# Performance work log

Hardware: AMD Instinct MI355X
Metric: run time of the kernel (lower is better)

## Reference

```python
import jax, jax.numpy as jnp
import numpy as np

BN_EPS = 1e-4  # KAIR BatchNorm2d eps


def conv1x1(x, W, b):
    # x: (b,c,h,w), W: (out,in), b: (out,)
    return jnp.einsum('oc,bchw->bohw', W, x) + b[None, :, None, None]


def setup_inputs() -> dict:
    key = jax.random.key(0)
    ks = jax.random.split(key, 16)
    b, c, h, w = 8, 64, 128, 128
    f32 = jnp.float32

    def rn(k, shape, s=0.05):
        return jax.random.normal(k, shape, f32) * s

    c3 = 3 * c
    return {
        'x': jax.random.normal(ks[0], (b, c, h, w), f32),
        'xf': jax.random.normal(ks[1], (b, c, h, w), f32),
        'xr': jax.random.normal(ks[2], (b, c, h, w), f32),
        'Wx': rn(ks[3], (c, c)), 'bx': jnp.zeros((c,), f32),
        'Wx1': rn(ks[4], (c, c)), 'bx1': jnp.zeros((c,), f32),
        'Wx2': rn(ks[5], (c, c)), 'bx2': jnp.zeros((c,), f32),
        'Wxf': rn(ks[6], (c, c)), 'bxf': jnp.zeros((c,), f32),
        'Wxr': rn(ks[7], (c, c)), 'bxr': jnp.zeros((c,), f32),
        'W_msa': rn(ks[8], (c3, c3, 3, 3)), 'b_msa': jnp.zeros((c3,), f32),
        'bn_gamma': jnp.ones((c3,), f32), 'bn_beta': jnp.zeros((c3,), f32),
        'bn_mean': jnp.zeros((c3,), f32), 'bn_var': jnp.ones((c3,), f32),
    }


def reference(x, xf, xr, Wx, bx, Wx1, bx1, Wx2, bx2, Wxf, bxf, Wxr, bxr,
              W_msa, b_msa, bn_gamma, bn_beta, bn_mean, bn_var):
    x_org = x
    # 1x1 conv projections (note: x1/x2 are projections of the projected x)
    xp = conv1x1(x, Wx, bx)
    x1 = conv1x1(xp, Wx1, bx1)
    x2 = conv1x1(xp, Wx2, bx2)
    xfp = conv1x1(xf, Wxf, bxf)
    xrp = conv1x1(xr, Wxr, bxr)

    # score1 = rearrange(x1,'b c h w->b h c w') @ rearrange(xf,'b c h w->b h w c') -> (b,h,c,c)
    score1 = jnp.einsum('bchw,bdhw->bhcd', x1, xfp)
    # feature_xf = score1 @ rearrange(x,'b c h w->b h c w'), rearranged back to (b,c,h,w)
    feature_xf = jnp.einsum('bhcd,bdhw->bchw', score1, xp)
    score2 = jnp.einsum('bchw,bdhw->bhcd', x2, xrp)
    feature_xr = jnp.einsum('bhcd,bdhw->bchw', score2, xp)

    out = jnp.concatenate([feature_xf, feature_xr, x_org], axis=1)  # (b,3c,h,w)
    # msa_conv: Conv2d(3c,3c,3,s=1,p=1) + BatchNorm2d(eval) + ReLU
    out = jax.lax.conv_general_dilated(
        out, W_msa, window_strides=(1, 1), padding='SAME',
        dimension_numbers=('NCHW', 'OIHW', 'NCHW'))
    out = out + b_msa[None, :, None, None]
    inv = jax.lax.rsqrt(bn_var + BN_EPS)
    out = (out - bn_mean[None, :, None, None]) * (bn_gamma * inv)[None, :, None, None] \
          + bn_beta[None, :, None, None]
    return jax.nn.relu(out)
```

## Files before the change

kernel.cpp:

```cpp
#include <hip/hip_runtime.h>

#define BATCH 8
#define C     64
#define H     128
#define WD    128
#define C3    192
#define HW    (H*WD)
#define PW    130
#define CBUF  (4*PW*64)

#define SWZ(r) ((((r) & 7) ^ (((r) >> 3) & 6)))

typedef __attribute__((ext_vector_type(8))) short short8;
typedef __attribute__((ext_vector_type(4))) float f32x4;
typedef unsigned short ushort_t;

__device__ __forceinline__ unsigned short f2bf(float f) {
    unsigned u = __builtin_bit_cast(unsigned, f);
    u += 0x7fffu + ((u >> 16) & 1u);
    return (unsigned short)(u >> 16);
}
__device__ __forceinline__ int pack2(unsigned short lo, unsigned short hi) {
    return (int)(((unsigned)hi << 16) | (unsigned)lo);
}

__global__ __launch_bounds__(64) void compose_kernel(
    const float* __restrict__ Wx,  const float* __restrict__ bx,
    const float* __restrict__ Wx1, const float* __restrict__ bx1,
    const float* __restrict__ Wx2, const float* __restrict__ bx2,
    const float* __restrict__ Wxf, const float* __restrict__ bxf,
    const float* __restrict__ Wxr, const float* __restrict__ bxr,
    ushort_t* __restrict__ Wall, float* __restrict__ ball)
{
    int o = blockIdx.x;
    int c = threadIdx.x;
    Wall[0*4096 + o*64 + c] = f2bf(Wx [o*64 + c]);
    Wall[3*4096 + o*64 + c] = f2bf(Wxf[o*64 + c]);
    Wall[4*4096 + o*64 + c] = f2bf(Wxr[o*64 + c]);
    float a1 = 0.f, a2 = 0.f;
    for (int k = 0; k < 64; ++k) {
        float wc = Wx[k*64 + c];
        a1 += Wx1[o*64 + k] * wc;
        a2 += Wx2[o*64 + k] * wc;
    }
    Wall[1*4096 + o*64 + c] = f2bf(a1);
    Wall[2*4096 + o*64 + c] = f2bf(a2);
    float t1 = Wx1[o*64 + c] * bx[c];
    float t2 = Wx2[o*64 + c] * bx[c];
    for (int off = 32; off; off >>= 1) {
        t1 += __shfl_down(t1, off);
        t2 += __shfl_down(t2, off);
    }
    if (c == 0) {
        ball[0*64 + o] = bx[o];
        ball[1*64 + o] = bx1[o] + t1;
        ball[2*64 + o] = bx2[o] + t2;
        ball[3*64 + o] = bxf[o];
        ball[4*64 + o] = bxr[o];
    }
}

__global__ __launch_bounds__(256) void prep_kernel(
    const float* __restrict__ x, const float* __restrict__ xf,
    const float* __restrict__ xr,
    ushort_t* __restrict__ xcl, ushort_t* __restrict__ feat,
    ushort_t* __restrict__ xfT, ushort_t* __restrict__ xrT)
{
    const int which = blockIdx.x / (BATCH*PW);
    const int r = blockIdx.x % (BATCH*PW);
    const int b = r / PW, py = r % PW;
    const int t = threadIdx.x;
    const size_t prow = ((size_t)b*PW + py)*PW;

    __shared__ ushort_t sx[128*72];

    if (which == 0) {
        if (py == 0 || py == PW-1) {
            int4 z = make_int4(0,0,0,0);
            for (int j = t; j < PW*128/8; j += 256) ((int4*)(feat + prow*128))[j] = z;
            for (int j = t; j < PW*64/8;  j += 256) ((int4*)(xcl  + prow*64 ))[j] = z;
            return;
        }
        if (t < 48) {
            int4 z = make_int4(0,0,0,0);
            if (t < 32) {
                int side = t >> 4, seg = t & 15;
                *(int4*)(feat + (prow + (side ? PW-1 : 0))*128 + seg*8) = z;
            } else {
                int u = t - 32, side = u >> 3, seg = u & 7;
                *(int4*)(xcl + (prow + (side ? PW-1 : 0))*64 + seg*8) = z;
            }
        }
        const int y = py - 1;
        for (int k = t; k < 64*128; k += 256) {
            int c = k >> 7, xx = k & 127;
            sx[xx*72 + c] = f2bf(x[((size_t)b*C + c)*HW + (size_t)y*WD + xx]);
        }
        __syncthreads();
        for (int j = t; j < 128*8; j += 256) {
            int xx = j >> 3, seg = j & 7;
            *(int4*)(xcl + (prow + xx + 1)*64 + seg*8) = *(const int4*)(sx + xx*72 + seg*8);
        }
        return;
    }

    if (py == 0 || py == PW-1) return;
    const int y = py - 1;
    const float* src = (which == 1) ? xf : xr;
    ushort_t* dstT   = (which == 1) ? xfT : xrT;
    for (int k = t; k < 64*128; k += 256) {
        int c = k >> 7, xx = k & 127;
        sx[xx*72 + c] = f2bf(src[((size_t)b*C + c)*HW + (size_t)y*WD + xx]);
    }
    __syncthreads();
    for (int j = t; j < 128*8; j += 256) {
        int xx = j >> 3, seg = j & 7;
        *(int4*)(dstT + (((size_t)b*128 + y)*128 + xx)*64 + seg*8) = *(const int4*)(sx + xx*72 + seg*8);
    }
}

__global__ __launch_bounds__(256, 3) void attn_mfma(
    const ushort_t* __restrict__ xcl, const ushort_t* __restrict__ xfT,
    const ushort_t* __restrict__ xrT,
    const ushort_t* __restrict__ Wall, const float* __restrict__ ball,
    ushort_t* __restrict__ feat)
{
    __shared__ ushort_t lds[6*4096];
    ushort_t* P = lds;
    ushort_t* Q = lds + 4096;
    ushort_t* U = lds + 2*4096;
    ushort_t* R = lds + 3*4096;
    ushort_t* V = lds + 4*4096;
    ushort_t* T = lds + 5*4096;

    const int t = threadIdx.x;
    const int wv = t >> 6, lane = t & 63, m = lane & 15, quad = lane >> 4;
    const int b = blockIdx.x >> 7, h = blockIdx.x & 127;
    const size_t rowbase = ((size_t)b*PW + h + 1)*PW;
    const ushort_t* xrow  = xcl + (rowbase + 1)*64;
    const ushort_t* xfrow = xfT + ((size_t)b*128 + h)*128*64;
    const ushort_t* xrrow = xrT + ((size_t)b*128 + h)*128*64;

    auto stageT = [&](const ushort_t* base, ushort_t* dst) {
#pragma unroll
        for (int it = 0; it < 2; ++it) {
            int slot = it*256 + t;
            int w = slot >> 3, seg = slot & 7;
            *(int4*)(dst + w*64 + ((seg ^ SWZ(w)) << 3)) =
                *(const int4*)(base + w*64 + seg*8);
        }
    };
    auto projB = [&](const ushort_t* src, const ushort_t* W, const float* bias,
                     ushort_t* dst) {
        int arow = wv*16 + m;
        int sa = SWZ(arow);
#pragma unroll
        for (int nt = 0; nt < 4; ++nt) {
            f32x4 acc = {0.f,0.f,0.f,0.f};
#pragma unroll
            for (int k = 0; k < 2; ++k) {
                short8 a  = *(const short8*)(src + arow*64 + (((4*k+quad) ^ sa) << 3));
                short8 bb = *(const short8*)(W   + (nt*16 + m)*64  + k*32 + quad*8);
                acc = __builtin_amdgcn_mfma_f32_16x16x32_bf16(a, bb, acc, 0,0,0);
            }
            float bo = bias[nt*16 + m];
            int o = nt*16 + m, w0 = wv*16 + quad*4;
            int base = o*64 + (((w0 >> 3) ^ SWZ(o)) << 3) + (w0 & 7);
            *(int*)(dst + base)     = pack2(f2bf(acc[0]+bo), f2bf(acc[1]+bo));
            *(int*)(dst + base + 2) = pack2(f2bf(acc[2]+bo), f2bf(acc[3]+bo));
        }
    };
    auto projA = [&](const ushort_t* src, const ushort_t* W, const float* bias,
                     ushort_t* dstT) {
        float b4[4];
#pragma unroll
        for (int r = 0; r < 4; ++r) b4[r] = bias[wv*16 + quad*4 + r];
#pragma unroll
        for (int nt = 0; nt < 4; ++nt) {
            f32x4 acc = {0.f,0.f,0.f,0.f};
            int brow = nt*16 + m;
            int sb = SWZ(brow);
#pragma unroll
            for (int k = 0; k < 2; ++k) {
                short8 a  = *(const short8*)(W   + (wv*16 + m)*64  + k*32 + quad*8);
                short8 bb = *(const short8*)(src + brow*64 + (((4*k+quad) ^ sb) << 3));
                acc = __builtin_amdgcn_mfma_f32_16x16x32_bf16(a, bb, acc, 0,0,0);
            }
            int w = nt*16 + m, o0 = wv*16 + quad*4;
            int base = w*64 + (((o0 >> 3) ^ SWZ(w)) << 3) + (o0 & 7);
            *(int*)(dstT + base)     = pack2(f2bf(acc[0]+b4[0]), f2bf(acc[1]+b4[1]));
            *(int*)(dstT + base + 2) = pack2(f2bf(acc[2]+b4[2]), f2bf(acc[3]+b4[3]));
        }
    };
    auto scoreStep = [&](const ushort_t* A, const ushort_t* B, f32x4* sc) {
        int arow = wv*16 + m;
        int sa = SWZ(arow);
#pragma unroll
        for (int nt = 0; nt < 4; ++nt) {
            int brow = nt*16 + m;
            int sb = SWZ(brow);
#pragma unroll
            for (int k = 0; k < 2; ++k) {
                short8 a  = *(const short8*)(A + arow*64 + (((4*k+quad) ^ sa) << 3));
                short8 bb = *(const short8*)(B + brow*64 + (((4*k+quad) ^ sb) << 3));
                sc[nt] = __builtin_amdgcn_mfma_f32_16x16x32_bf16(a, bb, sc[nt], 0,0,0);
            }
        }
    };
    auto scoreDump = [&](const f32x4* sc, ushort_t* dst) {
        int c0 = wv*16 + quad*4;
#pragma unroll
        for (int nt = 0; nt < 4; ++nt) {
            int d = nt*16 + m;
            int gd = d >> 3, dl = d & 7;
#pragma unroll
            for (int r = 0; r < 4; ++r) {
                int row = c0 + r;
                dst[row*64 + ((gd ^ SWZ(row)) << 3) + dl] = f2bf(sc[nt][r]);
            }
        }
    };
    auto featF = [&](const ushort_t* Sc, const ushort_t* XpT, ushort_t* stg) {
        int arow = wv*16 + m;
        int sa = SWZ(arow);
#pragma unroll
        for (int nt = 0; nt < 4; ++nt) {
            f32x4 acc = {0.f,0.f,0.f,0.f};
            int brow = nt*16 + m;
            int sb = SWZ(brow);
#pragma unroll
            for (int k = 0; k < 2; ++k) {
                short8 a  = *(const short8*)(Sc  + arow*64 + (((4*k+quad) ^ sa) << 3));
                short8 bb = *(const short8*)(XpT + brow*64 + (((4*k+quad) ^ sb) << 3));
                acc = __builtin_amdgcn_mfma_f32_16x16x32_bf16(a, bb, acc, 0,0,0);
            }
            int w = nt*16 + m, c0 = wv*16 + quad*4;
            int base = w*64 + (((c0 >> 3) ^ SWZ(w)) << 3) + (c0 & 7);
            *(int*)(stg + base)     = pack2(f2bf(acc[0]), f2bf(acc[1]));
            *(int*)(stg + base + 2) = pack2(f2bf(acc[2]), f2bf(acc[3]));
        }
    };
    auto emitPair = [&](const ushort_t* O1, const ushort_t* O2, int wc) {
#pragma unroll
        for (int it = 0; it < 4; ++it) {
            int j = (it & 1)*256 + t;
            const ushort_t* S = (it < 2) ? O1 : O2;
            int half = (it < 2) ? 0 : 64;
            int row = j >> 3, seg = j & 7;
            int4 v = *(const int4*)(S + row*64 + ((seg ^ SWZ(row)) << 3));
            *(int4*)(feat + (rowbase + wc + 1 + row)*128 + half + seg*8) = v;
        }
    };

    const ushort_t* W0 = Wall;            const float* b0 = ball;
    const ushort_t* W1 = Wall + 4096;     const float* b1 = ball + 64;
    const ushort_t* W2 = Wall + 2*4096;   const float* b2 = ball + 128;
    const ushort_t* W3 = Wall + 3*4096;   const float* b3 = ball + 192;
    const ushort_t* W4 = Wall + 4*4096;   const float* b4 = ball + 256;

    f32x4 sc1[4], sc2[4];
#pragma unroll
    for (int i = 0; i < 4; ++i) { sc1[i] = (f32x4){0,0,0,0}; sc2[i] = (f32x4){0,0,0,0}; }

    stageT(xrow, P); stageT(xfrow, Q); stageT(xrrow, U);
    __syncthreads();
    projB(P, W1, b1, R);  projB(P, W2, b2, V);  projB(Q, W3, b3, T);
    __syncthreads();
    scoreStep(R, T, sc1); projB(U, W4, b4, Q);
    __syncthreads();
    scoreStep(V, Q, sc2);
    stageT(xrow + 64*64, P); stageT(xfrow + 64*64, T); stageT(xrrow + 64*64, U);
    __syncthreads();
    projB(P, W1, b1, R);  projB(P, W2, b2, V);  projB(T, W3, b3, Q);
    __syncthreads();
    scoreStep(R, Q, sc1); projB(U, W4, b4, T);
    __syncthreads();
    scoreStep(V, T, sc2);
    stageT(xrow, P);
    __syncthreads();

    scoreDump(sc1, Q);  scoreDump(sc2, U);
    __syncthreads();
    projA(P, W0, b0, R);
    __syncthreads();
    featF(Q, R, P);  featF(U, R, T);  stageT(xrow + 64*64, V);
    __syncthreads();
    emitPair(P, T, 0);
    __syncthreads();
    projA(V, W0, b0, R);
    __syncthreads();
    featF(Q, R, V);  featF(U, R, T);
    __syncthreads();
    emitPair(V, T, 64);
}

__global__ __launch_bounds__(256) void pack_kernel(const float* __restrict__ W,
                                                   ushort_t* __restrict__ Wpk)
{
    int k = blockIdx.x*256 + threadIdx.x;
    if (k >= 12*54*64) return;
    int lane = k & 63, os = k >> 6;
    int otile = os / 54, s = os % 54;
    int tap = s / 6, icc = s % 6;
    int o   = otile*16 + (lane & 15);
    int ic0 = icc*32 + (lane >> 4)*8;
    ushort_t v[8];
#pragma unroll
    for (int j = 0; j < 8; ++j)
        v[j] = f2bf(W[(size_t)(o*C3 + ic0 + j)*9 + tap]);
    *(int4*)(Wpk + (size_t)k*8) = *(const int4*)v;
}

__global__ __launch_bounds__(512, 2) void conv_mfma(
    const ushort_t* __restrict__ feat, const ushort_t* __restrict__ xcl,
    const ushort_t* __restrict__ Wpk,
    const float* __restrict__ bias, const float* __restrict__ gamma,
    const float* __restrict__ beta, const float* __restrict__ mean,
    const float* __restrict__ var,  float* __restrict__ out)
{
    __shared__ ushort_t sA[2*CBUF];

    const int t = threadIdx.x;
    const int wv = t >> 6, lane = t & 63;
    const int m = lane & 15, quad = lane >> 4;
    const int b  = blockIdx.x >> 6, y0 = (blockIdx.x & 63)*2;
    const int yi = wv & 1, og = wv >> 1;

    f32x4 acc[24];
#pragma unroll
    for (int i = 0; i < 24; ++i) acc[i] = (f32x4){0.f,0.f,0.f,0.f};

    auto stageAll = [&](int ch, int bufi) {
        ushort_t* dst = sA + bufi*CBUF;
        const ushort_t* base = (ch < 2) ? feat : xcl;
        const int ps = (ch < 2) ? 128 : 64;
        const int co = (ch == 1) ? 64 : 0;
#pragma unroll
        for (int i = 0; i < 8; ++i) {
            int sl = i*512 + t;
            int wi = sl & 7, rowgx = sl >> 3;
            int row = rowgx / PW, gx = rowgx - row*PW;
            int wl = wi ^ (gx & 7);
            const ushort_t* g = base + (((size_t)b*PW + y0 + row)*PW + gx)*ps
                                     + co + wl*8;
            __builtin_amdgcn_global_load_lds(
                (const __attribute__((address_space(1))) unsigned int*)g,
                (__attribute__((address_space(3))) unsigned int*)(dst + (size_t)sl*8),
                16, 0, 0);
        }
        if (t < 64) {
            int sl = 4096 + t;
            int wi = sl & 7, rowgx = sl >> 3;
            int row = rowgx / PW, gx = rowgx - row*PW;
            int wl = wi ^ (gx & 7);
            const ushort_t* g = base + (((size_t)b*PW + y0 + row)*PW + gx)*ps
                                     + co + wl*8;
            __builtin_amdgcn_global_load_lds(
                (const __attribute__((address_space(1))) unsigned int*)g,
                (__attribute__((address_space(3))) unsigned int*)(dst + (size_t)sl*8),
                16, 0, 0);
        }
    };

    auto compute = [&](int ch, int bufi) {
        const ushort_t* src = sA + bufi*CBUF;
        short8 bf[6], bfn[6];
#pragma unroll
        for (int j = 0; j < 3; ++j)
#pragma unroll
            for (int k = 0; k < 2; ++k)
                bf[j*2+k] = *(const short8*)(Wpk +
                    (((size_t)(og*3+j)*54 + ch*2 + k)*64 + lane)*8);
#pragma unroll
        for (int tap = 0; tap < 9; ++tap) {
            if (tap < 8) {
#pragma unroll
                for (int j = 0; j < 3; ++j)
#pragma unroll
                    for (int k = 0; k < 2; ++k)
                        bfn[j*2+k] = *(const short8*)(Wpk +
                            (((size_t)(og*3+j)*54 + (tap+1)*6 + ch*2 + k)*64 + lane)*8);
            }
            const int ky = tap/3, kx = tap - ky*3;
            const int sw = (kx + m) & 7;
            const int rowb = ((yi + ky)*PW + kx + m)*64;
            const int g0 = (quad ^ sw)*8, g1 = ((quad+4) ^ sw)*8;
#pragma unroll
            for (int xt = 0; xt < 8; ++xt) {
                short8 af0 = *(const short8*)(src + rowb + xt*1024 + g0);
                short8 af1 = *(const short8*)(src + rowb + xt*1024 + g1);
#pragma unroll
                for (int j = 0; j < 3; ++j) {
                    acc[j*8+xt] = __builtin_amdgcn_mfma_f32_16x16x32_bf16(af0, bf[j*2],   acc[j*8+xt], 0,0,0);
                    acc[j*8+xt] = __builtin_amdgcn_mfma_f32_16x16x32_bf16(af1, bf[j*2+1], acc[j*8+xt], 0,0,0);
                }
            }
#pragma unroll
            for (int q = 0; q < 6; ++q) bf[q] = bfn[q];
        }
    };

    stageAll(0, 0);
    __syncthreads();
    for (int ch = 0; ch < 3; ++ch) {
        if (ch < 2) stageAll(ch + 1, (ch + 1) & 1);
        compute(ch, ch & 1);
        __syncthreads();
    }

    float* sOut = (float*)sA;
    for (int y = 0; y < 2; ++y) {
        if (yi == y) {
#pragma unroll
            for (int j = 0; j < 3; ++j) {
                int o = (og*3 + j)*16 + m;
                float A  = gamma[o] * rsqrtf(var[o] + 1e-4f);
                float Bv = (bias[o] - mean[o])*A + beta[o];
#pragma unroll
                for (int xt = 0; xt < 8; ++xt) {
                    f32x4 a4 = acc[j*8 + xt];
                    *(float4*)(sOut + o*132 + xt*16 + quad*4) =
                        make_float4(fmaxf(a4[0]*A + Bv, 0.f), fmaxf(a4[1]*A + Bv, 0.f),
                                    fmaxf(a4[2]*A + Bv, 0.f), fmaxf(a4[3]*A + Bv, 0.f));
                }
            }
        }
        __syncthreads();
#pragma unroll
        for (int i = 0; i < 12; ++i) {
            int s = i*512 + t;
            int o = s >> 5, xs4 = (s & 31)*4;
            float4 v = *(const float4*)(sOut + o*132 + xs4);
            *(float4*)(out + (((size_t)b*C3 + o)*H + y0 + y)*WD + xs4) = v;
        }
        __syncthreads();
    }
}

extern "C" void kernel_launch(void* const* d_in, const int* in_sizes, int n_in,
                              void* d_out, int out_size, void* d_ws, size_t ws_size,
                              hipStream_t stream)
{
    const float* x   = (const float*)d_in[0];
    const float* xf  = (const float*)d_in[1];
    const float* xr  = (const float*)d_in[2];
    const float* Wx  = (const float*)d_in[3];
    const float* bx  = (const float*)d_in[4];
    const float* Wx1 = (const float*)d_in[5];
    const float* bx1 = (const float*)d_in[6];
    const float* Wx2 = (const float*)d_in[7];
    const float* bx2 = (const float*)d_in[8];
    const float* Wxf = (const float*)d_in[9];
    const float* bxf = (const float*)d_in[10];
    const float* Wxr = (const float*)d_in[11];
    const float* bxr = (const float*)d_in[12];
    const float* Wm  = (const float*)d_in[13];
    const float* bms = (const float*)d_in[14];
    const float* gam = (const float*)d_in[15];
    const float* bet = (const float*)d_in[16];
    const float* mea = (const float*)d_in[17];
    const float* va  = (const float*)d_in[18];
    (void)in_sizes; (void)n_in; (void)out_size; (void)ws_size;

    ushort_t* feat = (ushort_t*)d_ws;
    ushort_t* xcl  = (ushort_t*)((char*)d_ws + 34611200);
    ushort_t* Wpk  = (ushort_t*)((char*)d_ws + 51916800);
    ushort_t* Wall = (ushort_t*)((char*)d_ws + 52700000);
    float*    ball = (float*)   ((char*)d_ws + 52750000);
    ushort_t* xfT  = (ushort_t*)d_out;
    ushort_t* xrT  = (ushort_t*)((char*)d_out + 16777216);
    float* outp = (float*)d_out;

    compose_kernel<<<dim3(64), dim3(64), 0, stream>>>(
        Wx, bx, Wx1, bx1, Wx2, bx2, Wxf, bxf, Wxr, bxr, Wall, ball);
    pack_kernel<<<dim3(162), dim3(256), 0, stream>>>(Wm, Wpk);
    prep_kernel<<<dim3(3*BATCH*PW), dim3(256), 0, stream>>>(
        x, xf, xr, xcl, feat, xfT, xrT);
    attn_mfma<<<dim3(BATCH*H), dim3(256), 0, stream>>>(
        xcl, xfT, xrT, Wall, ball, feat);
    conv_mfma<<<dim3(BATCH*64), dim3(512), 0, stream>>>(
        feat, xcl, Wpk, bms, gam, bet, mea, va, outp);
}
```

Before: 356.8 us.

## Split conv row tile into two x-halves to halve accumulators and LDS

The 3x3 conv MFMA kernel now processes each two-row tile in two 64-column halves. Each half stages a smaller halo buffer and keeps 12 accumulator vectors instead of 24. This cuts register and LDS use per block so more waves can be resident. In exchange, weights are reloaded twice per block, halo columns are restaged, and there are more barriers.

```diff
diff --git a/kernel.cpp b/kernel.cpp
--- a/kernel.cpp
+++ b/kernel.cpp
@@ -7,7 +7,8 @@
 #define C3    192
 #define HW    (H*WD)
 #define PW    130
-#define CBUF  (4*PW*64)
+#define HGX   66
+#define HBUF  (4*HGX*64)
 
 #define SWZ(r) ((((r) & 7) ^ (((r) >> 3) & 6)))
 
@@ -318,7 +319,7 @@
     const float* __restrict__ beta, const float* __restrict__ mean,
     const float* __restrict__ var,  float* __restrict__ out)
 {
-    __shared__ ushort_t sA[2*CBUF];
+    __shared__ ushort_t sA[2*HBUF];
 
     const int t = threadIdx.x;
     const int wv = t >> 6, lane = t & 63;
@@ -326,22 +327,20 @@
     const int b  = blockIdx.x >> 6, y0 = (blockIdx.x & 63)*2;
     const int yi = wv & 1, og = wv >> 1;
 
-    f32x4 acc[24];
-#pragma unroll
-    for (int i = 0; i < 24; ++i) acc[i] = (f32x4){0.f,0.f,0.f,0.f};
-
-    auto stageAll = [&](int ch, int bufi) {
-        ushort_t* dst = sA + bufi*CBUF;
+    f32x4 acc[12];
+
+    auto stageH = [&](int ch, int xh, int bufi) {
+        ushort_t* dst = sA + bufi*HBUF;
         const ushort_t* base = (ch < 2) ? feat : xcl;
         const int ps = (ch < 2) ? 128 : 64;
         const int co = (ch == 1) ? 64 : 0;
 #pragma unroll
-        for (int i = 0; i < 8; ++i) {
+        for (int i = 0; i < 4; ++i) {
             int sl = i*512 + t;
             int wi = sl & 7, rowgx = sl >> 3;
-            int row = rowgx / PW, gx = rowgx - row*PW;
-            int wl = wi ^ (gx & 7);
-            const ushort_t* g = base + (((size_t)b*PW + y0 + row)*PW + gx)*ps
+            int row = rowgx / HGX, gxl = rowgx - row*HGX;
+            int wl = wi ^ (gxl & 7);
+            const ushort_t* g = base + (((size_t)b*PW + y0 + row)*PW + xh*64 + gxl)*ps
                                      + co + wl*8;
             __builtin_amdgcn_global_load_lds(
                 (const __attribute__((address_space(1))) unsigned int*)g,
@@ -349,11 +348,11 @@
                 16, 0, 0);
         }
         if (t < 64) {
-            int sl = 4096 + t;
+            int sl = 2048 + t;
             int wi = sl & 7, rowgx = sl >> 3;
-            int row = rowgx / PW, gx = rowgx - row*PW;
-            int wl = wi ^ (gx & 7);
-            const ushort_t* g = base + (((size_t)b*PW + y0 + row)*PW + gx)*ps
+            int row = rowgx / HGX, gxl = rowgx - row*HGX;
+            int wl = wi ^ (gxl & 7);
+            const ushort_t* g = base + (((size_t)b*PW + y0 + row)*PW + xh*64 + gxl)*ps
                                      + co + wl*8;
             __builtin_amdgcn_global_load_lds(
                 (const __attribute__((address_space(1))) unsigned int*)g,
@@ -363,7 +362,7 @@
     };
 
     auto compute = [&](int ch, int bufi) {
-        const ushort_t* src = sA + bufi*CBUF;
+        const ushort_t* src = sA + bufi*HBUF;
         short8 bf[6], bfn[6];
 #pragma unroll
         for (int j = 0; j < 3; ++j)
@@ -383,16 +382,16 @@
             }
             const int ky = tap/3, kx = tap - ky*3;
             const int sw = (kx + m) & 7;
-            const int rowb = ((yi + ky)*PW + kx + m)*64;
+            const int rowb = ((yi + ky)*HGX + kx + m)*64;
             const int g0 = (quad ^ sw)*8, g1 = ((quad+4) ^ sw)*8;
 #pragma unroll
-            for (int xt = 0; xt < 8; ++xt) {
-                short8 af0 = *(const short8*)(src + rowb + xt*1024 + g0);
-                short8 af1 = *(const short8*)(src + rowb + xt*1024 + g1);
+            for (int xtl = 0; xtl < 4; ++xtl) {
+                short8 af0 = *(const short8*)(src + rowb + xtl*1024 + g0);
+                short8 af1 = *(const short8*)(src + rowb + xtl*1024 + g1);
 #pragma unroll
                 for (int j = 0; j < 3; ++j) {
-                    acc[j*8+xt] = __builtin_amdgcn_mfma_f32_16x16x32_bf16(af0, bf[j*2],   acc[j*8+xt], 0,0,0);
-                    acc[j*8+xt] = __builtin_amdgcn_mfma_f32_16x16x32_bf16(af1, bf[j*2+1], acc[j*8+xt], 0,0,0);
+                    acc[j*4+xtl] = __builtin_amdgcn_mfma_f32_16x16x32_bf16(af0, bf[j*2],   acc[j*4+xtl], 0,0,0);
+                    acc[j*4+xtl] = __builtin_amdgcn_mfma_f32_16x16x32_bf16(af1, bf[j*2+1], acc[j*4+xtl], 0,0,0);
                 }
             }
 #pragma unroll
@@ -400,40 +399,43 @@
         }
     };
 
-    stageAll(0, 0);
-    __syncthreads();
-    for (int ch = 0; ch < 3; ++ch) {
-        if (ch < 2) stageAll(ch + 1, (ch + 1) & 1);
-        compute(ch, ch & 1);
-        __syncthreads();
-    }
-
     float* sOut = (float*)sA;
-    for (int y = 0; y < 2; ++y) {
-        if (yi == y) {
-#pragma unroll
-            for (int j = 0; j < 3; ++j) {
-                int o = (og*3 + j)*16 + m;
-                float A  = gamma[o] * rsqrtf(var[o] + 1e-4f);
-                float Bv = (bias[o] - mean[o])*A + beta[o];
-#pragma unroll
-                for (int xt = 0; xt < 8; ++xt) {
-                    f32x4 a4 = acc[j*8 + xt];
-                    *(float4*)(sOut + o*132 + xt*16 + quad*4) =
-                        make_float4(fmaxf(a4[0]*A + Bv, 0.f), fmaxf(a4[1]*A + Bv, 0.f),
-                                    fmaxf(a4[2]*A + Bv, 0.f), fmaxf(a4[3]*A + Bv, 0.f));
+
+    for (int xh = 0; xh < 2; ++xh) {
+#pragma unroll
+        for (int i = 0; i < 12; ++i) acc[i] = (f32x4){0.f,0.f,0.f,0.f};
+
+        stageH(0, xh, 0);                 __syncthreads();
+        stageH(1, xh, 1);  compute(0, 0); __syncthreads();
+        stageH(2, xh, 0);  compute(1, 1); __syncthreads();
+                           compute(2, 0); __syncthreads();
+
+        for (int y = 0; y < 2; ++y) {
+            if (yi == y) {
+#pragma unroll
+                for (int j = 0; j < 3; ++j) {
+                    int o = (og*3 + j)*16 + m;
+                    float A  = gamma[o] * rsqrtf(var[o] + 1e-4f);
+                    float Bv = (bias[o] - mean[o])*A + beta[o];
+#pragma unroll
+                    for (int xtl = 0; xtl < 4; ++xtl) {
+                        f32x4 a4 = acc[j*4 + xtl];
+                        *(float4*)(sOut + o*68 + xtl*16 + quad*4) =
+                            make_float4(fmaxf(a4[0]*A + Bv, 0.f), fmaxf(a4[1]*A + Bv, 0.f),
+                                        fmaxf(a4[2]*A + Bv, 0.f), fmaxf(a4[3]*A + Bv, 0.f));
+                    }
                 }
             }
-        }
-        __syncthreads();
-#pragma unroll
-        for (int i = 0; i < 12; ++i) {
-            int s = i*512 + t;
-            int o = s >> 5, xs4 = (s & 31)*4;
-            float4 v = *(const float4*)(sOut + o*132 + xs4);
-            *(float4*)(out + (((size_t)b*C3 + o)*H + y0 + y)*WD + xs4) = v;
-        }
-        __syncthreads();
+            __syncthreads();
+#pragma unroll
+            for (int i = 0; i < 6; ++i) {
+                int s = i*512 + t;
+                int ol = s >> 4, xs4 = (s & 15)*4;
+                float4 v = *(const float4*)(sOut + ol*68 + xs4);
+                *(float4*)(out + (((size_t)b*C3 + ol)*H + y0 + y)*WD + xh*64 + xs4) = v;
+            }
+            __syncthreads();
+        }
     }
 }
 
```

Result: slower. 831.9 us (+133.2%).
